# Optimization experiments

Hardware: AMD Instinct MI355X
Metric: run time of the kernel (lower is better)

The kernel has to match this reference:

```python
import jax, jax.numpy as jnp
import numpy as np

ALP = 0.1
LAM = 1.0
N_NODES = 100000
N_EDGES = 800000
D_FEAT = 64


def setup_inputs() -> dict:
    key = jax.random.key(0)
    ks = jax.random.split(key, 7)
    h = jax.random.normal(ks[0], (N_NODES, D_FEAT), dtype=jnp.float32)
    ini_h = jax.random.normal(ks[1], (N_NODES, D_FEAT), dtype=jnp.float32)
    bef_A = jax.random.uniform(ks[2], (N_NODES, 1), dtype=jnp.float32)
    aft_A = jax.random.uniform(ks[3], (N_NODES, 1), dtype=jnp.float32)
    bef_X = jax.random.uniform(ks[4], (N_NODES, 1), dtype=jnp.float32)
    src = jax.random.randint(ks[5], (N_EDGES,), 0, N_NODES, dtype=jnp.int32)
    dst = jax.random.randint(ks[6], (N_EDGES,), 0, N_NODES, dtype=jnp.int32)
    return {"h": h, "ini_h": ini_h, "bef_A": bef_A, "aft_A": aft_A,
            "bef_X": bef_X, "src": src, "dst": dst}


def reference(h, ini_h, bef_A, aft_A, bef_X, src, dst):
    # propagation_lt:
    #   ini_h' = ini_h * bef_X
    #   agg    = A @ (h * aft_A)   (copy_u/sum over edges src->dst)
    #   out    = alp*lam * (agg * bef_A) + (1-alp)*h + alp*ini_h'
    pre_h = h
    msg = (h * aft_A)[src]                                  # [E, D]
    agg = jax.ops.segment_sum(msg, dst, num_segments=N_NODES)  # [N, D]
    agg = agg * bef_A
    return ALP * LAM * agg + (1.0 - ALP) * pre_h + ALP * (ini_h * bef_X)
```

## Files before the change

### kernel.cpp

```cpp
#include <hip/hip_runtime.h>

#define ALP 0.1f
#define OMA 0.9f
#define D 64
#define DV 16
#define SH 9
#define NODES_PER_B 512
#define CAP 16
#define OVF_MAX 65536

__device__ __forceinline__ unsigned short f2b(float f) {
    unsigned u = __float_as_uint(f);
    unsigned r = u + 0x7fffu + ((u >> 16) & 1u);
    return (unsigned short)(r >> 16);
}
__device__ __forceinline__ float b2f(unsigned short u) {
    return __uint_as_float(((unsigned)u) << 16);
}

__global__ __launch_bounds__(256) void vsgc_msgp1(
        const float4* __restrict__ h4, const float* __restrict__ aft_A,
        ushort4* __restrict__ msgb, int n16,
        const int4* __restrict__ src4, const int4* __restrict__ dst4,
        int* __restrict__ gcnt, int* __restrict__ buckets,
        int2* __restrict__ ovf, int* __restrict__ ovfCnt,
        int E, int NB, int BCAP, int p1Blocks) {
    int tid = threadIdx.x;
    if ((int)blockIdx.x >= p1Blocks) {
        int i = (blockIdx.x - p1Blocks) * 256 + tid;
        if (i < n16) {
            float w = aft_A[i >> 4];
            float4 v = h4[i];
            msgb[i] = make_ushort4(f2b(v.x * w), f2b(v.y * w), f2b(v.z * w), f2b(v.w * w));
        }
        return;
    }
    __shared__ int cnt[256], gbase[256], pos[256];
    cnt[tid] = 0; pos[tid] = 0;
    __syncthreads();
    int nInt4 = (E + 3) >> 2;
    int i0 = blockIdx.x * 512 + tid;
    int i1 = i0 + 256;
    bool v0 = i0 < nInt4, v1 = i1 < nInt4;
    int4 s0 = make_int4(0,0,0,0), d0 = s0, s1 = s0, d1 = s0;
    if (v0) { s0 = src4[i0]; d0 = dst4[i0]; }
    if (v1) { s1 = src4[i1]; d1 = dst4[i1]; }
    int e0 = i0 << 2, e1 = i1 << 2;
    int ss[8] = {s0.x, s0.y, s0.z, s0.w, s1.x, s1.y, s1.z, s1.w};
    int dd[8] = {d0.x, d0.y, d0.z, d0.w, d1.x, d1.y, d1.z, d1.w};
    bool ok[8];
#pragma unroll
    for (int k = 0; k < 4; ++k) { ok[k] = v0 && (e0 + k < E); ok[4 + k] = v1 && (e1 + k < E); }
#pragma unroll
    for (int k = 0; k < 8; ++k) if (ok[k]) atomicAdd(&cnt[dd[k] >> SH], 1);
    __syncthreads();
    if (tid < NB && cnt[tid] > 0) gbase[tid] = atomicAdd(&gcnt[tid], cnt[tid]);
    __syncthreads();
    int pp[8];
#pragma unroll
    for (int k = 0; k < 8; ++k)
        pp[k] = ok[k] ? (gbase[dd[k] >> SH] + atomicAdd(&pos[dd[k] >> SH], 1)) : 0;
#pragma unroll
    for (int k = 0; k < 8; ++k) {
        if (!ok[k]) continue;
        int b = dd[k] >> SH;
        int pkt = (ss[k] << SH) | (dd[k] & (NODES_PER_B - 1));
        if (pp[k] < BCAP) buckets[(size_t)b * BCAP + pp[k]] = pkt;
        else { int o = atomicAdd(ovfCnt, 1); if (o < OVF_MAX) ovf[o] = make_int2(ss[k], dd[k]); }
    }
}

__global__ __launch_bounds__(512) void p2_ell(const int* __restrict__ buckets,
                                              const int* __restrict__ gcnt,
                                              int* __restrict__ ell,
                                              int* __restrict__ cnt_g,
                                              int2* __restrict__ ovf,
                                              int* __restrict__ ovfCnt,
                                              int N, int BCAP) {
    __shared__ int npos[NODES_PER_B];
    int b = blockIdx.x, tid = threadIdx.x;
    npos[tid] = 0;
    __syncthreads();
    int nb = min(gcnt[b], BCAP);
    const int4* bp4 = (const int4*)(buckets + (size_t)b * BCAP);
    int nIter = (nb + 3) >> 2;
    for (int i4 = tid; i4 < nIter; i4 += 512) {
        int4 r4 = bp4[i4];
        int base = i4 << 2;
        int pk[4] = {r4.x, r4.y, r4.z, r4.w};
#pragma unroll
        for (int k = 0; k < 4; ++k) {
            if (base + k >= nb) break;
            int pkt = pk[k];
            int l = pkt & (NODES_PER_B - 1);
            int s = (int)(((unsigned)pkt) >> SH);
            int slot = atomicAdd(&npos[l], 1);
            int node = (b << SH) + l;
            if (slot < CAP) ell[(size_t)node * CAP + slot] = s;
            else { int o = atomicAdd(ovfCnt, 1); if (o < OVF_MAX) ovf[o] = make_int2(s, node); }
        }
    }
    __syncthreads();
    int node = (b << SH) + tid;
    if (node < N) cnt_g[node] = npos[tid];
}

__global__ __launch_bounds__(256) void vsgc_gather_ell(const ushort4* __restrict__ msgb,
                                                       const float4* __restrict__ h4,
                                                       const float4* __restrict__ ini4,
                                                       const float* __restrict__ bef_A,
                                                       const float* __restrict__ bef_X,
                                                       const int* __restrict__ cnt_g,
                                                       const int* __restrict__ ell,
                                                       float4* __restrict__ out4, int N) {
    int wid = (blockIdx.x * blockDim.x + threadIdx.x) >> 6;
    int g0 = wid * 2;
    if (g0 >= N) return;
    int g1 = g0 + 1;
    bool has1 = g1 < N;
    int g1c = has1 ? g1 : g0;
    int lane = threadIdx.x & 63;
    int w = lane >> 4;
    int q = lane & 15;
    size_t r0 = (size_t)g0 * DV + q;
    size_t r1 = (size_t)g1c * DV + q;
    int ev0 = ell[(size_t)g0 * CAP + q];
    int ev1 = ell[(size_t)g1c * CAP + q];
    int n0 = min(cnt_g[g0], CAP);
    int n1 = has1 ? min(cnt_g[g1c], CAP) : 0;
    float4 hv0 = h4[r0];
    float4 hv1 = h4[r1];
    float4 iv0 = ini4[r0];
    float4 iv1 = ini4[r1];
    float cb0 = ALP * bef_A[g0];
    float bx0 = ALP * bef_X[g0];
    float cb1 = ALP * bef_A[g1c];
    float bx1 = ALP * bef_X[g1c];
    float4 a0 = make_float4(0.f, 0.f, 0.f, 0.f);
    float4 a1 = a0;
    unsigned clampN = (unsigned)(N - 1);
#pragma unroll
    for (int k = 0; k < 4; ++k) {
        int idx = w + 4 * k;
        int s0 = __shfl(ev0, idx);
        int s1 = __shfl(ev1, idx);
        unsigned su0 = min((unsigned)s0, clampN);
        unsigned su1 = min((unsigned)s1, clampN);
        float m0 = (idx < n0) ? 1.f : 0.f;
        float m1 = (idx < n1) ? 1.f : 0.f;
        ushort4 q0 = msgb[(size_t)su0 * DV + q];
        ushort4 q1 = msgb[(size_t)su1 * DV + q];
        a0.x += m0 * b2f(q0.x); a0.y += m0 * b2f(q0.y);
        a0.z += m0 * b2f(q0.z); a0.w += m0 * b2f(q0.w);
        a1.x += m1 * b2f(q1.x); a1.y += m1 * b2f(q1.y);
        a1.z += m1 * b2f(q1.z); a1.w += m1 * b2f(q1.w);
    }
    a0.x += __shfl_xor(a0.x, 16); a0.y += __shfl_xor(a0.y, 16);
    a0.z += __shfl_xor(a0.z, 16); a0.w += __shfl_xor(a0.w, 16);
    a0.x += __shfl_xor(a0.x, 32); a0.y += __shfl_xor(a0.y, 32);
    a0.z += __shfl_xor(a0.z, 32); a0.w += __shfl_xor(a0.w, 32);
    a1.x += __shfl_xor(a1.x, 16); a1.y += __shfl_xor(a1.y, 16);
    a1.z += __shfl_xor(a1.z, 16); a1.w += __shfl_xor(a1.w, 16);
    a1.x += __shfl_xor(a1.x, 32); a1.y += __shfl_xor(a1.y, 32);
    a1.z += __shfl_xor(a1.z, 32); a1.w += __shfl_xor(a1.w, 32);
    if (w == 0) {
        float4 o;
        o.x = OMA * hv0.x + bx0 * iv0.x + cb0 * a0.x;
        o.y = OMA * hv0.y + bx0 * iv0.y + cb0 * a0.y;
        o.z = OMA * hv0.z + bx0 * iv0.z + cb0 * a0.z;
        o.w = OMA * hv0.w + bx0 * iv0.w + cb0 * a0.w;
        out4[r0] = o;
    } else if (w == 1 && has1) {
        float4 o;
        o.x = OMA * hv1.x + bx1 * iv1.x + cb1 * a1.x;
        o.y = OMA * hv1.y + bx1 * iv1.y + cb1 * a1.y;
        o.z = OMA * hv1.z + bx1 * iv1.z + cb1 * a1.z;
        o.w = OMA * hv1.w + bx1 * iv1.w + cb1 * a1.w;
        out4[r1] = o;
    }
}

__global__ void vsgc_ovf(const float4* __restrict__ h4,
                         const float* __restrict__ aft_A,
                         const float* __restrict__ bef_A,
                         const int2* __restrict__ ovf,
                         const int* __restrict__ ovfCnt,
                         float* __restrict__ out) {
    int total = min(*ovfCnt, OVF_MAX);
    int stride = blockDim.x * gridDim.x;
    for (int t = blockIdx.x * blockDim.x + threadIdx.x; t < total * 16; t += stride) {
        int e = t >> 4, q = t & 15;
        int2 r = ovf[e];
        float c = ALP * aft_A[r.x] * bef_A[r.y];
        float4 hv = h4[(size_t)r.x * DV + q];
        float* op = out + (size_t)r.y * D + (q << 2);
        unsafeAtomicAdd(op + 0, c * hv.x);
        unsafeAtomicAdd(op + 1, c * hv.y);
        unsafeAtomicAdd(op + 2, c * hv.z);
        unsafeAtomicAdd(op + 3, c * hv.w);
    }
}

__global__ void vsgc_init(const float4* __restrict__ h, const float4* __restrict__ ini_h,
                          const float* __restrict__ bef_X, float4* __restrict__ out, int n4) {
    int i = blockIdx.x * blockDim.x + threadIdx.x;
    if (i >= n4) return;
    int node = i >> 4;
    float bx = ALP * bef_X[node];
    float4 hv = h[i];
    float4 iv = ini_h[i];
    float4 o;
    o.x = OMA * hv.x + bx * iv.x;
    o.y = OMA * hv.y + bx * iv.y;
    o.z = OMA * hv.z + bx * iv.z;
    o.w = OMA * hv.w + bx * iv.w;
    out[i] = o;
}
__global__ void vsgc_edges_atomic(const float4* __restrict__ h,
                                  const float* __restrict__ aft_A,
                                  const float* __restrict__ bef_A,
                                  const int* __restrict__ src,
                                  const int* __restrict__ dst,
                                  float* __restrict__ out, int E) {
    int tid = blockIdx.x * blockDim.x + threadIdx.x;
    int e = tid >> 4;
    int q = tid & 15;
    if (e >= E) return;
    int s = src[e];
    int d = dst[e];
    float c = ALP * aft_A[s] * bef_A[d];
    float4 hv = h[(size_t)s * DV + q];
    float* op = out + (size_t)d * D + (q << 2);
    unsafeAtomicAdd(op + 0, c * hv.x);
    unsafeAtomicAdd(op + 1, c * hv.y);
    unsafeAtomicAdd(op + 2, c * hv.z);
    unsafeAtomicAdd(op + 3, c * hv.w);
}

extern "C" void kernel_launch(void* const* d_in, const int* in_sizes, int n_in,
                              void* d_out, int out_size, void* d_ws, size_t ws_size,
                              hipStream_t stream) {
    const float* h     = (const float*)d_in[0];
    const float* ini_h = (const float*)d_in[1];
    const float* bef_A = (const float*)d_in[2];
    const float* aft_A = (const float*)d_in[3];
    const float* bef_X = (const float*)d_in[4];
    const int*   src   = (const int*)d_in[5];
    const int*   dst   = (const int*)d_in[6];
    float* out = (float*)d_out;

    const int N = in_sizes[0] / D;
    const int E = in_sizes[5];
    const int t = 256;

    int NB = (N + NODES_PER_B - 1) >> SH;
    int perB = (NB > 0) ? E / NB : 0;
    int BCAP = ((perB + perB / 4 + 256) + 3) & ~3;

    size_t o_gcnt = 0;
    size_t o_ovfc = 256 * 4;
    size_t o_ovf  = ((o_ovfc + 64 * 4 + 255) / 256) * 256;
    size_t o_cnt  = o_ovf + (size_t)OVF_MAX * 8;
    size_t o_ell  = ((o_cnt + (size_t)N * 4 + 255) / 256) * 256;
    size_t o_bkt  = ((o_ell + (size_t)N * CAP * 4 + 255) / 256) * 256;
    size_t o_msg  = ((o_bkt + (size_t)NB * BCAP * 4 + 255) / 256) * 256;
    size_t need   = o_msg + (size_t)N * 128;

    if (NB <= 256 && N <= (1 << (31 - SH)) && ws_size >= need) {
        int*  gcnt  = (int*)((char*)d_ws + o_gcnt);
        int*  ovfC  = (int*)((char*)d_ws + o_ovfc);
        int2* ovf   = (int2*)((char*)d_ws + o_ovf);
        int*  cnt_g = (int*)((char*)d_ws + o_cnt);
        int*  ell   = (int*)((char*)d_ws + o_ell);
        int*  bkt   = (int*)((char*)d_ws + o_bkt);
        ushort4* msgb = (ushort4*)((char*)d_ws + o_msg);

        hipMemsetAsync(d_ws, 0, o_ovf, stream);

        int n16 = N * DV;
        int nInt4 = (E + 3) >> 2;
        int p1Blocks = (nInt4 + 511) / 512;
        int msgBlocks = (n16 + t - 1) / t;
        vsgc_msgp1<<<p1Blocks + msgBlocks, t, 0, stream>>>(
            (const float4*)h, aft_A, msgb, n16,
            (const int4*)src, (const int4*)dst, gcnt, bkt, ovf, ovfC,
            E, NB, BCAP, p1Blocks);

        p2_ell<<<NB, 512, 0, stream>>>(bkt, gcnt, ell, cnt_g, ovf, ovfC, N, BCAP);

        long long waves = (N + 1) / 2;
        long long threadsTotal = waves * 64;
        vsgc_gather_ell<<<(int)((threadsTotal + t - 1) / t), t, 0, stream>>>(
            msgb, (const float4*)h, (const float4*)ini_h, bef_A, bef_X,
            cnt_g, ell, (float4*)out, N);

        vsgc_ovf<<<32, t, 0, stream>>>((const float4*)h, aft_A, bef_A, ovf, ovfC, out);
    } else {
        int n4 = N * DV;
        vsgc_init<<<(n4 + t - 1) / t, t, 0, stream>>>(
            (const float4*)h, (const float4*)ini_h, bef_X, (float4*)out, n4);
        long long total = (long long)E * DV;
        vsgc_edges_atomic<<<(int)((total + t - 1) / t), t, 0, stream>>>(
            (const float4*)h, aft_A, bef_A, src, dst, out, E);
    }
}
```

Measured before the change: 159.1 us.

## Fuse ELL build and gather into per-bucket shared-memory atomic aggregation

Replaces the ELL construction kernel and the separate gather kernel with one kernel per 256-node bucket. Each block accumulates bf16 messages into a 64KB shared-memory float tile using LDS atomics with a rotated component order to spread bank conflicts, then writes the fused output epilogue. This removes the ELL write/read round trip, the per-node degree cap, and one launch. In exchange there are only about 391 large blocks with high LDS use, so occupancy is low, and LDS atomics may contend.

```diff
diff --git a/kernel.cpp b/kernel.cpp
--- a/kernel.cpp
+++ b/kernel.cpp
@@ -4,9 +4,9 @@
 #define OMA 0.9f
 #define D 64
 #define DV 16
-#define SH 9
-#define NODES_PER_B 512
-#define CAP 16
+#define SH 8
+#define NODES_PER_B 256
+#define NBMAX 512
 #define OVF_MAX 65536
 
 __device__ __forceinline__ unsigned short f2b(float f) {
@@ -35,8 +35,9 @@
         }
         return;
     }
-    __shared__ int cnt[256], gbase[256], pos[256];
-    cnt[tid] = 0; pos[tid] = 0;
+    __shared__ int cnt[NBMAX], gbase[NBMAX], pos[NBMAX];
+    cnt[tid] = 0; cnt[tid + 256] = 0;
+    pos[tid] = 0; pos[tid + 256] = 0;
     __syncthreads();
     int nInt4 = (E + 3) >> 2;
     int i0 = blockIdx.x * 512 + tid;
@@ -54,7 +55,8 @@
 #pragma unroll
     for (int k = 0; k < 8; ++k) if (ok[k]) atomicAdd(&cnt[dd[k] >> SH], 1);
     __syncthreads();
-    if (tid < NB && cnt[tid] > 0) gbase[tid] = atomicAdd(&gcnt[tid], cnt[tid]);
+    for (int bb = tid; bb < NB; bb += 256)
+        if (cnt[bb] > 0) gbase[bb] = atomicAdd(&gcnt[bb], cnt[bb]);
     __syncthreads();
     int pp[8];
 #pragma unroll
@@ -70,113 +72,58 @@
     }
 }
 
-__global__ __launch_bounds__(512) void p2_ell(const int* __restrict__ buckets,
-                                              const int* __restrict__ gcnt,
-                                              int* __restrict__ ell,
-                                              int* __restrict__ cnt_g,
-                                              int2* __restrict__ ovf,
-                                              int* __restrict__ ovfCnt,
-                                              int N, int BCAP) {
-    __shared__ int npos[NODES_PER_B];
+__global__ __launch_bounds__(512) void p2_agg(
+        const int* __restrict__ buckets, const int* __restrict__ gcnt,
+        const ushort4* __restrict__ msgb,
+        const float4* __restrict__ h4, const float4* __restrict__ ini4,
+        const float* __restrict__ bef_A, const float* __restrict__ bef_X,
+        float4* __restrict__ out4, int N, int BCAP) {
+    __shared__ float acc[NODES_PER_B * D];
     int b = blockIdx.x, tid = threadIdx.x;
-    npos[tid] = 0;
+    for (int i = tid; i < NODES_PER_B * D; i += 512) acc[i] = 0.f;
     __syncthreads();
     int nb = min(gcnt[b], BCAP);
-    const int4* bp4 = (const int4*)(buckets + (size_t)b * BCAP);
-    int nIter = (nb + 3) >> 2;
-    for (int i4 = tid; i4 < nIter; i4 += 512) {
-        int4 r4 = bp4[i4];
-        int base = i4 << 2;
-        int pk[4] = {r4.x, r4.y, r4.z, r4.w};
-#pragma unroll
-        for (int k = 0; k < 4; ++k) {
-            if (base + k >= nb) break;
-            int pkt = pk[k];
-            int l = pkt & (NODES_PER_B - 1);
-            int s = (int)(((unsigned)pkt) >> SH);
-            int slot = atomicAdd(&npos[l], 1);
-            int node = (b << SH) + l;
-            if (slot < CAP) ell[(size_t)node * CAP + slot] = s;
-            else { int o = atomicAdd(ovfCnt, 1); if (o < OVF_MAX) ovf[o] = make_int2(s, node); }
+    const int* bp = buckets + (size_t)b * BCAP;
+    int lane = tid & 63;
+    int w = tid >> 6;
+    int sub = lane >> 4;
+    int q = lane & 15;
+    for (int base = w * 4; base < nb; base += 32) {
+        int e = base + sub;
+        bool act = e < nb;
+        int ec = act ? e : (nb - 1);
+        int pkt = bp[ec];
+        int s = (int)(((unsigned)pkt) >> SH);
+        int l = pkt & (NODES_PER_B - 1);
+        ushort4 m = msgb[(size_t)s * DV + q];
+        if (act) {
+            float* ap = acc + l * D + (q << 2);
+            int r = l & 3;
+            atomicAdd(&ap[r],           b2f(m.x));
+            atomicAdd(&ap[(1 + r) & 3], b2f(m.y));
+            atomicAdd(&ap[(2 + r) & 3], b2f(m.z));
+            atomicAdd(&ap[(3 + r) & 3], b2f(m.w));
         }
     }
     __syncthreads();
-    int node = (b << SH) + tid;
-    if (node < N) cnt_g[node] = npos[tid];
-}
-
-__global__ __launch_bounds__(256) void vsgc_gather_ell(const ushort4* __restrict__ msgb,
-                                                       const float4* __restrict__ h4,
-                                                       const float4* __restrict__ ini4,
-                                                       const float* __restrict__ bef_A,
-                                                       const float* __restrict__ bef_X,
-                                                       const int* __restrict__ cnt_g,
-                                                       const int* __restrict__ ell,
-                                                       float4* __restrict__ out4, int N) {
-    int wid = (blockIdx.x * blockDim.x + threadIdx.x) >> 6;
-    int g0 = wid * 2;
-    if (g0 >= N) return;
-    int g1 = g0 + 1;
-    bool has1 = g1 < N;
-    int g1c = has1 ? g1 : g0;
-    int lane = threadIdx.x & 63;
-    int w = lane >> 4;
-    int q = lane & 15;
-    size_t r0 = (size_t)g0 * DV + q;
-    size_t r1 = (size_t)g1c * DV + q;
-    int ev0 = ell[(size_t)g0 * CAP + q];
-    int ev1 = ell[(size_t)g1c * CAP + q];
-    int n0 = min(cnt_g[g0], CAP);
-    int n1 = has1 ? min(cnt_g[g1c], CAP) : 0;
-    float4 hv0 = h4[r0];
-    float4 hv1 = h4[r1];
-    float4 iv0 = ini4[r0];
-    float4 iv1 = ini4[r1];
-    float cb0 = ALP * bef_A[g0];
-    float bx0 = ALP * bef_X[g0];
-    float cb1 = ALP * bef_A[g1c];
-    float bx1 = ALP * bef_X[g1c];
-    float4 a0 = make_float4(0.f, 0.f, 0.f, 0.f);
-    float4 a1 = a0;
-    unsigned clampN = (unsigned)(N - 1);
-#pragma unroll
-    for (int k = 0; k < 4; ++k) {
-        int idx = w + 4 * k;
-        int s0 = __shfl(ev0, idx);
-        int s1 = __shfl(ev1, idx);
-        unsigned su0 = min((unsigned)s0, clampN);
-        unsigned su1 = min((unsigned)s1, clampN);
-        float m0 = (idx < n0) ? 1.f : 0.f;
-        float m1 = (idx < n1) ? 1.f : 0.f;
-        ushort4 q0 = msgb[(size_t)su0 * DV + q];
-        ushort4 q1 = msgb[(size_t)su1 * DV + q];
-        a0.x += m0 * b2f(q0.x); a0.y += m0 * b2f(q0.y);
-        a0.z += m0 * b2f(q0.z); a0.w += m0 * b2f(q0.w);
-        a1.x += m1 * b2f(q1.x); a1.y += m1 * b2f(q1.y);
-        a1.z += m1 * b2f(q1.z); a1.w += m1 * b2f(q1.w);
-    }
-    a0.x += __shfl_xor(a0.x, 16); a0.y += __shfl_xor(a0.y, 16);
-    a0.z += __shfl_xor(a0.z, 16); a0.w += __shfl_xor(a0.w, 16);
-    a0.x += __shfl_xor(a0.x, 32); a0.y += __shfl_xor(a0.y, 32);
-    a0.z += __shfl_xor(a0.z, 32); a0.w += __shfl_xor(a0.w, 32);
-    a1.x += __shfl_xor(a1.x, 16); a1.y += __shfl_xor(a1.y, 16);
-    a1.z += __shfl_xor(a1.z, 16); a1.w += __shfl_xor(a1.w, 16);
-    a1.x += __shfl_xor(a1.x, 32); a1.y += __shfl_xor(a1.y, 32);
-    a1.z += __shfl_xor(a1.z, 32); a1.w += __shfl_xor(a1.w, 32);
-    if (w == 0) {
+    int node0 = b << SH;
+    for (int i = tid; i < NODES_PER_B * DV; i += 512) {
+        int l = i >> 4, qq = i & 15;
+        int node = node0 + l;
+        if (node >= N) continue;
+        float cb = ALP * bef_A[node];
+        float bx = ALP * bef_X[node];
+        size_t rr = (size_t)node * DV + qq;
+        float4 hv = h4[rr];
+        float4 iv = ini4[rr];
+        const float* ap = acc + l * D + (qq << 2);
+        int r = l & 3;
         float4 o;
-        o.x = OMA * hv0.x + bx0 * iv0.x + cb0 * a0.x;
-        o.y = OMA * hv0.y + bx0 * iv0.y + cb0 * a0.y;
-        o.z = OMA * hv0.z + bx0 * iv0.z + cb0 * a0.z;
-        o.w = OMA * hv0.w + bx0 * iv0.w + cb0 * a0.w;
-        out4[r0] = o;
-    } else if (w == 1 && has1) {
-        float4 o;
-        o.x = OMA * hv1.x + bx1 * iv1.x + cb1 * a1.x;
-        o.y = OMA * hv1.y + bx1 * iv1.y + cb1 * a1.y;
-        o.z = OMA * hv1.z + bx1 * iv1.z + cb1 * a1.z;
-        o.w = OMA * hv1.w + bx1 * iv1.w + cb1 * a1.w;
-        out4[r1] = o;
+        o.x = OMA * hv.x + bx * iv.x + cb * ap[r];
+        o.y = OMA * hv.y + bx * iv.y + cb * ap[(1 + r) & 3];
+        o.z = OMA * hv.z + bx * iv.z + cb * ap[(2 + r) & 3];
+        o.w = OMA * hv.w + bx * iv.w + cb * ap[(3 + r) & 3];
+        out4[rr] = o;
     }
 }
 
@@ -258,20 +205,16 @@
     int BCAP = ((perB + perB / 4 + 256) + 3) & ~3;
 
     size_t o_gcnt = 0;
-    size_t o_ovfc = 256 * 4;
+    size_t o_ovfc = NBMAX * 4;
     size_t o_ovf  = ((o_ovfc + 64 * 4 + 255) / 256) * 256;
-    size_t o_cnt  = o_ovf + (size_t)OVF_MAX * 8;
-    size_t o_ell  = ((o_cnt + (size_t)N * 4 + 255) / 256) * 256;
-    size_t o_bkt  = ((o_ell + (size_t)N * CAP * 4 + 255) / 256) * 256;
+    size_t o_bkt  = ((o_ovf + (size_t)OVF_MAX * 8 + 255) / 256) * 256;
     size_t o_msg  = ((o_bkt + (size_t)NB * BCAP * 4 + 255) / 256) * 256;
     size_t need   = o_msg + (size_t)N * 128;
 
-    if (NB <= 256 && N <= (1 << (31 - SH)) && ws_size >= need) {
+    if (NB <= NBMAX && N <= (1 << (31 - SH)) && ws_size >= need) {
         int*  gcnt  = (int*)((char*)d_ws + o_gcnt);
         int*  ovfC  = (int*)((char*)d_ws + o_ovfc);
         int2* ovf   = (int2*)((char*)d_ws + o_ovf);
-        int*  cnt_g = (int*)((char*)d_ws + o_cnt);
-        int*  ell   = (int*)((char*)d_ws + o_ell);
         int*  bkt   = (int*)((char*)d_ws + o_bkt);
         ushort4* msgb = (ushort4*)((char*)d_ws + o_msg);
 
@@ -286,13 +229,9 @@
             (const int4*)src, (const int4*)dst, gcnt, bkt, ovf, ovfC,
             E, NB, BCAP, p1Blocks);
 
-        p2_ell<<<NB, 512, 0, stream>>>(bkt, gcnt, ell, cnt_g, ovf, ovfC, N, BCAP);
-
-        long long waves = (N + 1) / 2;
-        long long threadsTotal = waves * 64;
-        vsgc_gather_ell<<<(int)((threadsTotal + t - 1) / t), t, 0, stream>>>(
-            msgb, (const float4*)h, (const float4*)ini_h, bef_A, bef_X,
-            cnt_g, ell, (float4*)out, N);
+        p2_agg<<<NB, 512, 0, stream>>>(
+            bkt, gcnt, msgb, (const float4*)h, (const float4*)ini_h,
+            bef_A, bef_X, (float4*)out, N, BCAP);
 
         vsgc_ovf<<<32, t, 0, stream>>>((const float4*)h, aft_A, bef_A, ovf, ovfC, out);
     } else {
```

After: 472.9 us. 197% more time.

## Fuse ELL build into gather kernel using shared-memory ELL per bucket

Applied to the files above, without the earlier changes.

Merges the bucket-to-ELL kernel and the gather kernel into one, keeping each bucket's ELL adjacency and counts in shared memory rather than writing them to global memory and reading them back. To keep the per-block shared footprint small and the block count high, buckets shrink from 512 to 128 nodes, which raises the bucket count to about 782 and needs larger shared histograms in the first pass. This saves one launch and a global ELL round trip. In exchange, each block now loops over 64 node pairs with 8 waves, so the gather phase gets less parallelism per launch than the old one-wave-per-pair grid.

```diff
diff --git a/kernel.cpp b/kernel.cpp
--- a/kernel.cpp
+++ b/kernel.cpp
@@ -4,8 +4,9 @@
 #define OMA 0.9f
 #define D 64
 #define DV 16
-#define SH 9
-#define NODES_PER_B 512
+#define SH 7
+#define NODES_PER_B 128
+#define NBMAX 1024
 #define CAP 16
 #define OVF_MAX 65536
 
@@ -35,8 +36,9 @@
         }
         return;
     }
-    __shared__ int cnt[256], gbase[256], pos[256];
-    cnt[tid] = 0; pos[tid] = 0;
+    __shared__ int cnt[NBMAX], gbase[NBMAX], pos[NBMAX];
+#pragma unroll
+    for (int j = 0; j < NBMAX / 256; ++j) { cnt[tid + j * 256] = 0; pos[tid + j * 256] = 0; }
     __syncthreads();
     int nInt4 = (E + 3) >> 2;
     int i0 = blockIdx.x * 512 + tid;
@@ -54,7 +56,8 @@
 #pragma unroll
     for (int k = 0; k < 8; ++k) if (ok[k]) atomicAdd(&cnt[dd[k] >> SH], 1);
     __syncthreads();
-    if (tid < NB && cnt[tid] > 0) gbase[tid] = atomicAdd(&gcnt[tid], cnt[tid]);
+    for (int bb = tid; bb < NB; bb += 256)
+        if (cnt[bb] > 0) gbase[bb] = atomicAdd(&gcnt[bb], cnt[bb]);
     __syncthreads();
     int pp[8];
 #pragma unroll
@@ -70,16 +73,17 @@
     }
 }
 
-__global__ __launch_bounds__(512) void p2_ell(const int* __restrict__ buckets,
-                                              const int* __restrict__ gcnt,
-                                              int* __restrict__ ell,
-                                              int* __restrict__ cnt_g,
-                                              int2* __restrict__ ovf,
-                                              int* __restrict__ ovfCnt,
-                                              int N, int BCAP) {
+__global__ __launch_bounds__(512) void p2_gather(
+        const int* __restrict__ buckets, const int* __restrict__ gcnt,
+        const ushort4* __restrict__ msgb,
+        const float4* __restrict__ h4, const float4* __restrict__ ini4,
+        const float* __restrict__ bef_A, const float* __restrict__ bef_X,
+        int2* __restrict__ ovf, int* __restrict__ ovfCnt,
+        float4* __restrict__ out4, int N, int BCAP) {
     __shared__ int npos[NODES_PER_B];
+    __shared__ int ells[NODES_PER_B * CAP];
     int b = blockIdx.x, tid = threadIdx.x;
-    npos[tid] = 0;
+    if (tid < NODES_PER_B) npos[tid] = 0;
     __syncthreads();
     int nb = min(gcnt[b], BCAP);
     const int4* bp4 = (const int4*)(buckets + (size_t)b * BCAP);
@@ -95,88 +99,80 @@
             int l = pkt & (NODES_PER_B - 1);
             int s = (int)(((unsigned)pkt) >> SH);
             int slot = atomicAdd(&npos[l], 1);
-            int node = (b << SH) + l;
-            if (slot < CAP) ell[(size_t)node * CAP + slot] = s;
-            else { int o = atomicAdd(ovfCnt, 1); if (o < OVF_MAX) ovf[o] = make_int2(s, node); }
-        }
-    }
-    __syncthreads();
-    int node = (b << SH) + tid;
-    if (node < N) cnt_g[node] = npos[tid];
-}
-
-__global__ __launch_bounds__(256) void vsgc_gather_ell(const ushort4* __restrict__ msgb,
-                                                       const float4* __restrict__ h4,
-                                                       const float4* __restrict__ ini4,
-                                                       const float* __restrict__ bef_A,
-                                                       const float* __restrict__ bef_X,
-                                                       const int* __restrict__ cnt_g,
-                                                       const int* __restrict__ ell,
-                                                       float4* __restrict__ out4, int N) {
-    int wid = (blockIdx.x * blockDim.x + threadIdx.x) >> 6;
-    int g0 = wid * 2;
-    if (g0 >= N) return;
-    int g1 = g0 + 1;
-    bool has1 = g1 < N;
-    int g1c = has1 ? g1 : g0;
-    int lane = threadIdx.x & 63;
+            if (slot < CAP) ells[l * CAP + slot] = s;
+            else { int o = atomicAdd(ovfCnt, 1); if (o < OVF_MAX) ovf[o] = make_int2(s, (b << SH) + l); }
+        }
+    }
+    __syncthreads();
+    int lane = tid & 63;
+    int wv = tid >> 6;
     int w = lane >> 4;
     int q = lane & 15;
-    size_t r0 = (size_t)g0 * DV + q;
-    size_t r1 = (size_t)g1c * DV + q;
-    int ev0 = ell[(size_t)g0 * CAP + q];
-    int ev1 = ell[(size_t)g1c * CAP + q];
-    int n0 = min(cnt_g[g0], CAP);
-    int n1 = has1 ? min(cnt_g[g1c], CAP) : 0;
-    float4 hv0 = h4[r0];
-    float4 hv1 = h4[r1];
-    float4 iv0 = ini4[r0];
-    float4 iv1 = ini4[r1];
-    float cb0 = ALP * bef_A[g0];
-    float bx0 = ALP * bef_X[g0];
-    float cb1 = ALP * bef_A[g1c];
-    float bx1 = ALP * bef_X[g1c];
-    float4 a0 = make_float4(0.f, 0.f, 0.f, 0.f);
-    float4 a1 = a0;
+    int node0 = b << SH;
     unsigned clampN = (unsigned)(N - 1);
-#pragma unroll
-    for (int k = 0; k < 4; ++k) {
-        int idx = w + 4 * k;
-        int s0 = __shfl(ev0, idx);
-        int s1 = __shfl(ev1, idx);
-        unsigned su0 = min((unsigned)s0, clampN);
-        unsigned su1 = min((unsigned)s1, clampN);
-        float m0 = (idx < n0) ? 1.f : 0.f;
-        float m1 = (idx < n1) ? 1.f : 0.f;
-        ushort4 q0 = msgb[(size_t)su0 * DV + q];
-        ushort4 q1 = msgb[(size_t)su1 * DV + q];
-        a0.x += m0 * b2f(q0.x); a0.y += m0 * b2f(q0.y);
-        a0.z += m0 * b2f(q0.z); a0.w += m0 * b2f(q0.w);
-        a1.x += m1 * b2f(q1.x); a1.y += m1 * b2f(q1.y);
-        a1.z += m1 * b2f(q1.z); a1.w += m1 * b2f(q1.w);
-    }
-    a0.x += __shfl_xor(a0.x, 16); a0.y += __shfl_xor(a0.y, 16);
-    a0.z += __shfl_xor(a0.z, 16); a0.w += __shfl_xor(a0.w, 16);
-    a0.x += __shfl_xor(a0.x, 32); a0.y += __shfl_xor(a0.y, 32);
-    a0.z += __shfl_xor(a0.z, 32); a0.w += __shfl_xor(a0.w, 32);
-    a1.x += __shfl_xor(a1.x, 16); a1.y += __shfl_xor(a1.y, 16);
-    a1.z += __shfl_xor(a1.z, 16); a1.w += __shfl_xor(a1.w, 16);
-    a1.x += __shfl_xor(a1.x, 32); a1.y += __shfl_xor(a1.y, 32);
-    a1.z += __shfl_xor(a1.z, 32); a1.w += __shfl_xor(a1.w, 32);
-    if (w == 0) {
-        float4 o;
-        o.x = OMA * hv0.x + bx0 * iv0.x + cb0 * a0.x;
-        o.y = OMA * hv0.y + bx0 * iv0.y + cb0 * a0.y;
-        o.z = OMA * hv0.z + bx0 * iv0.z + cb0 * a0.z;
-        o.w = OMA * hv0.w + bx0 * iv0.w + cb0 * a0.w;
-        out4[r0] = o;
-    } else if (w == 1 && has1) {
-        float4 o;
-        o.x = OMA * hv1.x + bx1 * iv1.x + cb1 * a1.x;
-        o.y = OMA * hv1.y + bx1 * iv1.y + cb1 * a1.y;
-        o.z = OMA * hv1.z + bx1 * iv1.z + cb1 * a1.z;
-        o.w = OMA * hv1.w + bx1 * iv1.w + cb1 * a1.w;
-        out4[r1] = o;
+    for (int pair = wv; pair < NODES_PER_B / 2; pair += 8) {
+        int l0 = pair * 2;
+        int g0 = node0 + l0;
+        if (g0 >= N) break;
+        int g1 = g0 + 1;
+        bool has1 = g1 < N;
+        int l1c = has1 ? (l0 + 1) : l0;
+        int g1c = node0 + l1c;
+        size_t r0 = (size_t)g0 * DV + q;
+        size_t r1 = (size_t)g1c * DV + q;
+        int ev0 = ells[l0 * CAP + q];
+        int ev1 = ells[l1c * CAP + q];
+        int n0 = min(npos[l0], CAP);
+        int n1 = has1 ? min(npos[l1c], CAP) : 0;
+        float4 hv0 = h4[r0];
+        float4 hv1 = h4[r1];
+        float4 iv0 = ini4[r0];
+        float4 iv1 = ini4[r1];
+        float cb0 = ALP * bef_A[g0];
+        float bx0 = ALP * bef_X[g0];
+        float cb1 = ALP * bef_A[g1c];
+        float bx1 = ALP * bef_X[g1c];
+        float4 a0 = make_float4(0.f, 0.f, 0.f, 0.f);
+        float4 a1 = a0;
+#pragma unroll
+        for (int k = 0; k < 4; ++k) {
+            int idx = w + 4 * k;
+            int s0 = __shfl(ev0, idx);
+            int s1 = __shfl(ev1, idx);
+            unsigned su0 = min((unsigned)s0, clampN);
+            unsigned su1 = min((unsigned)s1, clampN);
+            float m0 = (idx < n0) ? 1.f : 0.f;
+            float m1 = (idx < n1) ? 1.f : 0.f;
+            ushort4 q0 = msgb[(size_t)su0 * DV + q];
+            ushort4 q1 = msgb[(size_t)su1 * DV + q];
+            a0.x += m0 * b2f(q0.x); a0.y += m0 * b2f(q0.y);
+            a0.z += m0 * b2f(q0.z); a0.w += m0 * b2f(q0.w);
+            a1.x += m1 * b2f(q1.x); a1.y += m1 * b2f(q1.y);
+            a1.z += m1 * b2f(q1.z); a1.w += m1 * b2f(q1.w);
+        }
+        a0.x += __shfl_xor(a0.x, 16); a0.y += __shfl_xor(a0.y, 16);
+        a0.z += __shfl_xor(a0.z, 16); a0.w += __shfl_xor(a0.w, 16);
+        a0.x += __shfl_xor(a0.x, 32); a0.y += __shfl_xor(a0.y, 32);
+        a0.z += __shfl_xor(a0.z, 32); a0.w += __shfl_xor(a0.w, 32);
+        a1.x += __shfl_xor(a1.x, 16); a1.y += __shfl_xor(a1.y, 16);
+        a1.z += __shfl_xor(a1.z, 16); a1.w += __shfl_xor(a1.w, 16);
+        a1.x += __shfl_xor(a1.x, 32); a1.y += __shfl_xor(a1.y, 32);
+        a1.z += __shfl_xor(a1.z, 32); a1.w += __shfl_xor(a1.w, 32);
+        if (w == 0) {
+            float4 o;
+            o.x = OMA * hv0.x + bx0 * iv0.x + cb0 * a0.x;
+            o.y = OMA * hv0.y + bx0 * iv0.y + cb0 * a0.y;
+            o.z = OMA * hv0.z + bx0 * iv0.z + cb0 * a0.z;
+            o.w = OMA * hv0.w + bx0 * iv0.w + cb0 * a0.w;
+            out4[r0] = o;
+        } else if (w == 1 && has1) {
+            float4 o;
+            o.x = OMA * hv1.x + bx1 * iv1.x + cb1 * a1.x;
+            o.y = OMA * hv1.y + bx1 * iv1.y + cb1 * a1.y;
+            o.z = OMA * hv1.z + bx1 * iv1.z + cb1 * a1.z;
+            o.w = OMA * hv1.w + bx1 * iv1.w + cb1 * a1.w;
+            out4[r1] = o;
+        }
     }
 }
 
@@ -258,20 +254,16 @@
     int BCAP = ((perB + perB / 4 + 256) + 3) & ~3;
 
     size_t o_gcnt = 0;
-    size_t o_ovfc = 256 * 4;
+    size_t o_ovfc = NBMAX * 4;
     size_t o_ovf  = ((o_ovfc + 64 * 4 + 255) / 256) * 256;
-    size_t o_cnt  = o_ovf + (size_t)OVF_MAX * 8;
-    size_t o_ell  = ((o_cnt + (size_t)N * 4 + 255) / 256) * 256;
-    size_t o_bkt  = ((o_ell + (size_t)N * CAP * 4 + 255) / 256) * 256;
+    size_t o_bkt  = ((o_ovf + (size_t)OVF_MAX * 8 + 255) / 256) * 256;
     size_t o_msg  = ((o_bkt + (size_t)NB * BCAP * 4 + 255) / 256) * 256;
     size_t need   = o_msg + (size_t)N * 128;
 
-    if (NB <= 256 && N <= (1 << (31 - SH)) && ws_size >= need) {
+    if (NB <= NBMAX && N <= (1 << (31 - SH)) && ws_size >= need) {
         int*  gcnt  = (int*)((char*)d_ws + o_gcnt);
         int*  ovfC  = (int*)((char*)d_ws + o_ovfc);
         int2* ovf   = (int2*)((char*)d_ws + o_ovf);
-        int*  cnt_g = (int*)((char*)d_ws + o_cnt);
-        int*  ell   = (int*)((char*)d_ws + o_ell);
         int*  bkt   = (int*)((char*)d_ws + o_bkt);
         ushort4* msgb = (ushort4*)((char*)d_ws + o_msg);
 
@@ -286,13 +278,9 @@
             (const int4*)src, (const int4*)dst, gcnt, bkt, ovf, ovfC,
             E, NB, BCAP, p1Blocks);
 
-        p2_ell<<<NB, 512, 0, stream>>>(bkt, gcnt, ell, cnt_g, ovf, ovfC, N, BCAP);
-
-        long long waves = (N + 1) / 2;
-        long long threadsTotal = waves * 64;
-        vsgc_gather_ell<<<(int)((threadsTotal + t - 1) / t), t, 0, stream>>>(
-            msgb, (const float4*)h, (const float4*)ini_h, bef_A, bef_X,
-            cnt_g, ell, (float4*)out, N);
+        p2_gather<<<NB, 512, 0, stream>>>(
+            bkt, gcnt, msgb, (const float4*)h, (const float4*)ini_h,
+            bef_A, bef_X, ovf, ovfC, (float4*)out, N, BCAP);
 
         vsgc_ovf<<<32, t, 0, stream>>>((const float4*)h, aft_A, bef_A, ovf, ovfC, out);
     } else {
```

Result: slower. 164.7 us (+3.5%).
